# Kernel optimization log

Hardware: AMD Instinct MI355X
Metric: run time of the kernel (lower is better)

Reference implementation:

```python
import jax, jax.numpy as jnp
import numpy as np

B, S, D = 4, 2048, 1024  # batch, seq_len, input_dimension
KD, VD = 1024, 1024      # key_dim, value_dim


def setup_inputs() -> dict:
    key = jax.random.key(0)
    ks = jax.random.split(key, 9)
    sc_in = 1.0 / np.sqrt(D)
    sc_v = 1.0 / np.sqrt(VD)
    return {
        "x":  jax.random.normal(ks[0], (B, S, D), dtype=jnp.float32),
        "Wq": jax.random.normal(ks[1], (KD, D), dtype=jnp.float32) * sc_in,
        "bq": jax.random.normal(ks[2], (KD,), dtype=jnp.float32) * 0.01,
        "Wk": jax.random.normal(ks[3], (KD, D), dtype=jnp.float32) * sc_in,
        "bk": jax.random.normal(ks[4], (KD,), dtype=jnp.float32) * 0.01,
        "Wv": jax.random.normal(ks[5], (VD, D), dtype=jnp.float32) * sc_in,
        "bv": jax.random.normal(ks[6], (VD,), dtype=jnp.float32) * 0.01,
        "Wo": jax.random.normal(ks[7], (D, VD), dtype=jnp.float32) * sc_v,
        "bo": jax.random.normal(ks[8], (D,), dtype=jnp.float32) * 0.01,
    }


def reference(x, Wq, bq, Wk, bk, Wv, bv, Wo, bo):
    # projections (torch Linear: x @ W.T + b)
    q = jnp.einsum('bsd,kd->bsk', x, Wq) + bq   # (B,S,KD)
    k = jnp.einsum('bsd,kd->bsk', x, Wk) + bk   # (B,S,KD)
    v = jnp.einsum('bsd,vd->bsv', x, Wv) + bv   # (B,S,VD)

    scores = jnp.einsum('bqk,bsk->bqs', q, k) / jnp.sqrt(jnp.float32(KD))  # (B,S,S)

    # sign rescale: scores * sign(scores) (sign(0) mapped to 1) == |scores| with zeros kept
    sign_mask = jnp.sign(scores)
    sign_mask = sign_mask + (sign_mask == 0).astype(jnp.float32)

    # causal mask: lower-triangular (incl diag) multiplied by 1, strict upper -> -inf
    seq = scores.shape[-1]
    causal = jnp.tril(jnp.ones((seq, seq), dtype=bool))
    masked = jnp.where(causal, scores * sign_mask, -jnp.inf)

    weights = jax.nn.softmax(masked, axis=2)            # (B,S,S)
    out = jnp.einsum('bqs,bsv->bqv', weights, v)        # (B,S,VD)
    return jnp.einsum('bqv,dv->bqd', out, Wo) + bo      # (B,S,D)
```

## Files before the change

### kernel.cpp

```cpp
#include <hip/hip_runtime.h>
#include <hip/hip_bf16.h>
#include <cstdint>


#define BM 128
#define BN 128

typedef __attribute__((ext_vector_type(8))) __bf16 bf16x8;
typedef __attribute__((ext_vector_type(4))) __bf16 bf16x4;
typedef __attribute__((ext_vector_type(4))) float floatx4;

struct WPtr3 { const __bf16* w[3]; };
struct BPtr3 { const float* b[3]; };
struct Ptr3 { const float* p[3]; };

__device__ __forceinline__ void async_copy16(const __bf16* g, const __bf16* l) {
  __builtin_amdgcn_global_load_lds(
      (const __attribute__((address_space(1))) unsigned int*)(const void*)g,
      (__attribute__((address_space(3))) unsigned int*)(unsigned)(uintptr_t)(const void*)l,
      16, 0, 0);
}

__device__ __forceinline__ void gemm_core(const __bf16* __restrict__ pA,
                                          const __bf16* __restrict__ pB,
                                          int K, int kSteps64, int mb, int nb,
                                          floatx4 (&acc)[4][4]) {
  __shared__ __align__(16) __bf16 As0[BM * 32];
  __shared__ __align__(16) __bf16 As1[BM * 32];
  __shared__ __align__(16) __bf16 Bs0[BN * 32];
  __shared__ __align__(16) __bf16 Bs1[BN * 32];

  const int t = threadIdx.x;
  const int lane = t & 63;
  const int wave = t >> 6;
  const int quad = lane >> 4;
  const int l16 = lane & 15;
  const int wm = wave >> 1;
  const int wn = wave & 1;

  const __bf16* gA = pA + (long)(mb * BM + (t >> 2)) * K + ((t & 3) * 8);
  const __bf16* gB = pB + (long)(nb * BN + (t >> 2)) * K + ((t & 3) * 8);
  const long rowHalf = (long)64 * K;
  __bf16* lA0 = &As0[t * 8];
  __bf16* lA1 = &As1[t * 8];
  __bf16* lB0 = &Bs0[t * 8];
  __bf16* lB1 = &Bs1[t * 8];

  for (int kk = 0; kk < kSteps64; ++kk) {
    const long ko = (long)kk * 64;
    async_copy16(gA + ko, lA0);
    async_copy16(gA + ko + rowHalf, lA0 + 2048);
    async_copy16(gA + ko + 32, lA1);
    async_copy16(gA + ko + 32 + rowHalf, lA1 + 2048);
    async_copy16(gB + ko, lB0);
    async_copy16(gB + ko + rowHalf, lB0 + 2048);
    async_copy16(gB + ko + 32, lB1);
    async_copy16(gB + ko + 32 + rowHalf, lB1 + 2048);
    __syncthreads();

#pragma unroll
    for (int p = 0; p < 2; ++p) {
      const __bf16* As = p ? As1 : As0;
      const __bf16* Bs = p ? Bs1 : Bs0;
      bf16x8 af[4], bfr[4];
#pragma unroll
      for (int i = 0; i < 4; ++i) {
        af[i] = *(const bf16x8*)&As[(wm * 64 + i * 16 + l16) * 32 + quad * 8];
        bfr[i] = *(const bf16x8*)&Bs[(wn * 64 + i * 16 + l16) * 32 + quad * 8];
      }
#pragma unroll
      for (int i = 0; i < 4; ++i)
#pragma unroll
        for (int j = 0; j < 4; ++j)
          acc[i][j] = __builtin_amdgcn_mfma_f32_16x16x32_bf16(af[i], bfr[j],
                                                              acc[i][j], 0, 0, 0);
    }
    __syncthreads();
  }
}

__global__ void __launch_bounds__(256, 2)
gemm_wvo(const __bf16* __restrict__ Wob, const __bf16* __restrict__ Wvt,
         __bf16* __restrict__ Wvo) {
  const int id = blockIdx.x;
  const int mb = id >> 3, nb = id & 7;
  floatx4 acc[4][4] = {};
  gemm_core(Wob, Wvt, 1024, 16, mb, nb, acc);

  const int t = threadIdx.x;
  const int lane = t & 63, wave = t >> 6;
  const int rb = (wave >> 1) * 64 + (lane >> 4) * 4;
  const int cb = (wave & 1) * 64 + (lane & 15);
#pragma unroll
  for (int j4 = 0; j4 < 4; ++j4) {
    const int gc = nb * BN + cb + j4 * 16;
#pragma unroll
    for (int i = 0; i < 4; ++i) {
      const int gr = mb * BM + rb + i * 16;
#pragma unroll
      for (int r = 0; r < 4; ++r)
        Wvo[(long)(gr + r) * 1024 + gc] = (__bf16)acc[i][j4][r];
    }
  }
}

__global__ void __launch_bounds__(256, 2)
gemm_qku(const __bf16* __restrict__ xb, WPtr3 wgt, BPtr3 bias,
         __bf16* __restrict__ qk, __bf16* __restrict__ Ut,
         int S, int D, int KD, int B) {
  const int id = blockIdx.x;
  const int xcd = id & 7;
  const int j = id >> 3;
  const int mb = xcd * 8 + (j & 7);
  const int rest = j >> 3;
  const int nb = rest & 7;
  const int z = rest >> 3;

  floatx4 acc[4][4] = {};
  gemm_core(xb, wgt.w[z], D, D / 64, mb, nb, acc);

  const int t = threadIdx.x;
  const int lane = t & 63, wave = t >> 6;
  const int rb = (wave >> 1) * 64 + (lane >> 4) * 4;
  const int cb = (wave & 1) * 64 + (lane & 15);
  const float* bz = bias.b[z];

  if (z < 2) {
    __bf16* C = qk + (long)z * B * S * KD;
#pragma unroll
    for (int j4 = 0; j4 < 4; ++j4) {
      const int gc = nb * BN + cb + j4 * 16;
      const float bv = bz[gc];
#pragma unroll
      for (int i = 0; i < 4; ++i) {
        const int gr = mb * BM + rb + i * 16;
#pragma unroll
        for (int r = 0; r < 4; ++r)
          C[(long)(gr + r) * KD + gc] = (__bf16)(acc[i][j4][r] + bv);
      }
    }
  } else {
    const int bb = (mb * BM) / S;
    const int s0 = mb * BM - bb * S;
#pragma unroll
    for (int j4 = 0; j4 < 4; ++j4) {
      const int gc = nb * BN + cb + j4 * 16;
      const float bv = bz[gc];
#pragma unroll
      for (int i = 0; i < 4; ++i) {
        const int sr = s0 + rb + i * 16;
        bf16x4 o;
#pragma unroll
        for (int r = 0; r < 4; ++r) o[r] = (__bf16)(acc[i][j4][r] + bv);
        *(bf16x4*)&Ut[((long)bb * D + gc) * S + sr] = o;
      }
    }
  }
}

__global__ void __launch_bounds__(256, 2)
gemm_scores(const __bf16* __restrict__ q, const __bf16* __restrict__ k,
            __bf16* __restrict__ P, float* __restrict__ lsum, int S, int KD) {
  const int id = blockIdx.x;
  const int xcd = id & 7;
  const int j = id >> 3;
  const int nb = j & 15;
  const int comb = j >> 4;
  const int b = comb >> 1;
  const int mb = (comb & 1) ? (15 - xcd) : xcd;
  if (nb > mb) return;

  floatx4 acc[4][4] = {};
  gemm_core(q + (long)b * S * KD, k + (long)b * S * KD, KD, KD / 64, mb, nb, acc);

  const int t = threadIdx.x;
  const int lane = t & 63, wave = t >> 6;
  const int l16 = lane & 15;
  const int rb = (wave >> 1) * 64 + (lane >> 4) * 4;
  const int cb = (wave & 1) * 64 + l16;
  __bf16* C = P + (long)b * S * S;
  float* lrow = lsum + (long)b * S;
  const float sc = 0.03125f;

#pragma unroll
  for (int i = 0; i < 4; ++i) {
#pragma unroll
    for (int r = 0; r < 4; ++r) {
      const int row = mb * BM + rb + i * 16 + r;
      float psum = 0.f;
#pragma unroll
      for (int j4 = 0; j4 < 4; ++j4) {
        const int col = nb * BN + cb + j4 * 16;
        const float p = (col <= row) ? __expf(fabsf(acc[i][j4][r] * sc)) : 0.f;
        psum += p;
        C[(long)row * S + col] = (__bf16)p;
      }
      psum += __shfl_xor(psum, 1, 64);
      psum += __shfl_xor(psum, 2, 64);
      psum += __shfl_xor(psum, 4, 64);
      psum += __shfl_xor(psum, 8, 64);
      if (l16 == 0) atomicAdd(&lrow[row], psum);
    }
  }
}

__global__ void __launch_bounds__(256, 2)
gemm_pvo(const __bf16* __restrict__ P, const __bf16* __restrict__ Ut,
         const float* __restrict__ lsum, const float* __restrict__ bo,
         float* __restrict__ out, int S, int D) {
  const int id = blockIdx.x;
  const int xcd = id & 7;
  const int j = id >> 3;
  const int nb = j & 7;
  const int comb = j >> 3;
  const int b = comb >> 1;
  const int mb = (comb & 1) ? (15 - xcd) : xcd;

  floatx4 acc[4][4] = {};
  gemm_core(P + (long)b * S * S, Ut + (long)b * D * S, S, (mb + 1) * 2, mb, nb,
            acc);

  const int t = threadIdx.x;
  const int lane = t & 63, wave = t >> 6;
  const int rb = (wave >> 1) * 64 + (lane >> 4) * 4;
  const int cb = (wave & 1) * 64 + (lane & 15);
  const float* lrow = lsum + (long)b * S;

#pragma unroll
  for (int i = 0; i < 4; ++i) {
#pragma unroll
    for (int r = 0; r < 4; ++r) {
      const int row = mb * BM + rb + i * 16 + r;
      const float inv = 1.f / lrow[row];
#pragma unroll
      for (int j4 = 0; j4 < 4; ++j4) {
        const int col = nb * BN + cb + j4 * 16;
        out[((long)b * S + row) * D + col] = acc[i][j4][r] * inv + bo[col];
      }
    }
  }
}

__global__ void prep(const float* __restrict__ x, Ptr3 wp,
                     const float* __restrict__ Wv, const float* __restrict__ bv,
                     __bf16* __restrict__ xb, __bf16* __restrict__ Wb,
                     __bf16* __restrict__ Wvt, float* __restrict__ bvo,
                     float* __restrict__ lsum) {
  __shared__ __bf16 tile[64][66];
  __shared__ float wsum[4];
  const int bid = blockIdx.x;
  const int t = threadIdx.x;
  if (bid < 8192) {
    const long i = ((long)bid * 256 + t) * 4;
    const float4 f = *(const float4*)(x + i);
    bf16x4 o;
    o[0] = (__bf16)f.x; o[1] = (__bf16)f.y; o[2] = (__bf16)f.z; o[3] = (__bf16)f.w;
    *(bf16x4*)(xb + i) = o;
  } else if (bid < 11264) {
    const int slot = (bid - 8192) * 256 + t;
    const int which = slot >> 18;
    const long e = (long)(slot & 0x3ffff) * 4;
    const float4 f = *(const float4*)(wp.p[which] + e);
    bf16x4 o;
    o[0] = (__bf16)f.x; o[1] = (__bf16)f.y; o[2] = (__bf16)f.z; o[3] = (__bf16)f.w;
    *(bf16x4*)(Wb + ((long)which << 20) + e) = o;
  } else if (bid < 11520) {
    const int idx = bid - 11264;
    const int r0 = (idx >> 4) * 64, c0 = (idx & 15) * 64;
#pragma unroll
    for (int e = 0; e < 16; ++e) {
      const int i = e * 256 + t;
      const int r = i >> 6, c = i & 63;
      tile[r][c] = (__bf16)Wv[(long)(r0 + r) * 1024 + (c0 + c)];
    }
    __syncthreads();
#pragma unroll
    for (int e = 0; e < 16; ++e) {
      const int i = e * 256 + t;
      const int r = i >> 6, c = i & 63;
      Wvt[(long)(c0 + r) * 1024 + (r0 + c)] = tile[c][r];
    }
  } else if (bid < 12544) {
    const int d = bid - 11520;
    const float* row = wp.p[2] + (long)d * 1024;
    float s = 0.f;
    for (int v = t; v < 1024; v += 256) s += bv[v] * row[v];
#pragma unroll
    for (int off = 32; off > 0; off >>= 1) s += __shfl_down(s, off, 64);
    if ((t & 63) == 0) wsum[t >> 6] = s;
    __syncthreads();
    if (t == 0) bvo[d] = wsum[0] + wsum[1] + wsum[2] + wsum[3];
  } else {
#pragma unroll
    for (int e = 0; e < 8; ++e)
      *(float4*)(lsum + (e * 256 + t) * 4) = float4{0.f, 0.f, 0.f, 0.f};
  }
}

extern "C" void kernel_launch(void* const* d_in, const int* in_sizes, int n_in,
                              void* d_out, int out_size, void* d_ws, size_t ws_size,
                              hipStream_t stream) {
  const float* x = (const float*)d_in[0];
  const float* Wq = (const float*)d_in[1];
  const float* bq = (const float*)d_in[2];
  const float* Wk = (const float*)d_in[3];
  const float* bk = (const float*)d_in[4];
  const float* Wv = (const float*)d_in[5];
  const float* bv = (const float*)d_in[6];
  const float* Wo = (const float*)d_in[7];
  const float* bo = (const float*)d_in[8];
  float* out = (float*)d_out;

  constexpr int B = 4, S = 2048, D = 1024, KD = 1024;
  constexpr long MB_ = 1024 * 1024;

  char* w = (char*)d_ws;
  __bf16* xb = (__bf16*)(w);
  __bf16* qk = (__bf16*)(w + 16 * MB_);
  __bf16* Ut = (__bf16*)(w + 48 * MB_);
  __bf16* P  = (__bf16*)(w + 64 * MB_);
  __bf16* Wb = (__bf16*)(w + 96 * MB_);
  __bf16* Wvt = (__bf16*)(w + 102 * MB_);
  __bf16* Wvo = (__bf16*)(w + 104 * MB_);
  float* lsum = (float*)(w + 106 * MB_);
  float* bvo = (float*)(w + 106 * MB_ + 65536);

  __bf16* Wqb = Wb;
  __bf16* Wkb = Wb + (1l << 20);
  __bf16* Wob = Wb + (2l << 20);

  Ptr3 wp{{Wq, Wk, Wo}};
  prep<<<12545, 256, 0, stream>>>(x, wp, Wv, bv, xb, Wb, Wvt, bvo, lsum);

  gemm_wvo<<<64, 256, 0, stream>>>(Wob, Wvt, Wvo);

  WPtr3 w3{{Wqb, Wkb, Wvo}};
  BPtr3 b3{{bq, bk, bvo}};
  gemm_qku<<<1536, 256, 0, stream>>>(xb, w3, b3, qk, Ut, S, D, KD, B);

  gemm_scores<<<1024, 256, 0, stream>>>(qk, qk + (long)B * S * KD, P, lsum, S, KD);

  gemm_pvo<<<512, 256, 0, stream>>>(P, Ut, lsum, bo, out, S, D);
}
```

Before: 261.0 us.

## Split-K the causal PV·Wo GEMM into fixed-size K chunks with atomic accumulation

The final P×(V·Wo) GEMM previously gave each block a K range proportional to its row-block index, so causal triangular work was badly imbalanced across 512 blocks. It now splits K into chunks of 8 steps (512 columns), launching 1280 blocks that each handle one chunk and atomically add partial results into a zeroed output, with the bias added only by the first chunk. This adds a memset of the output and fp32 atomic traffic, and makes the summation order nondeterministic.

Result: slower. 320.0 us (+22.6%).

```diff
diff --git a/kernel.cpp b/kernel.cpp
--- a/kernel.cpp
+++ b/kernel.cpp
@@ -23,8 +23,8 @@
 
 __device__ __forceinline__ void gemm_core(const __bf16* __restrict__ pA,
                                           const __bf16* __restrict__ pB,
-                                          int K, int kSteps64, int mb, int nb,
-                                          floatx4 (&acc)[4][4]) {
+                                          int K, int kBeg, int kEnd, int mb,
+                                          int nb, floatx4 (&acc)[4][4]) {
   __shared__ __align__(16) __bf16 As0[BM * 32];
   __shared__ __align__(16) __bf16 As1[BM * 32];
   __shared__ __align__(16) __bf16 Bs0[BN * 32];
@@ -46,7 +46,7 @@
   __bf16* lB0 = &Bs0[t * 8];
   __bf16* lB1 = &Bs1[t * 8];
 
-  for (int kk = 0; kk < kSteps64; ++kk) {
+  for (int kk = kBeg; kk < kEnd; ++kk) {
     const long ko = (long)kk * 64;
     async_copy16(gA + ko, lA0);
     async_copy16(gA + ko + rowHalf, lA0 + 2048);
@@ -85,7 +85,7 @@
   const int id = blockIdx.x;
   const int mb = id >> 3, nb = id & 7;
   floatx4 acc[4][4] = {};
-  gemm_core(Wob, Wvt, 1024, 16, mb, nb, acc);
+  gemm_core(Wob, Wvt, 1024, 0, 16, mb, nb, acc);
 
   const int t = threadIdx.x;
   const int lane = t & 63, wave = t >> 6;
@@ -117,7 +117,7 @@
   const int z = rest >> 3;
 
   floatx4 acc[4][4] = {};
-  gemm_core(xb, wgt.w[z], D, D / 64, mb, nb, acc);
+  gemm_core(xb, wgt.w[z], D, 0, D / 64, mb, nb, acc);
 
   const int t = threadIdx.x;
   const int lane = t & 63, wave = t >> 6;
@@ -171,7 +171,8 @@
   if (nb > mb) return;
 
   floatx4 acc[4][4] = {};
-  gemm_core(q + (long)b * S * KD, k + (long)b * S * KD, KD, KD / 64, mb, nb, acc);
+  gemm_core(q + (long)b * S * KD, k + (long)b * S * KD, KD, 0, KD / 64, mb, nb,
+            acc);
 
   const int t = threadIdx.x;
   const int lane = t & 63, wave = t >> 6;
@@ -211,13 +212,18 @@
   const int id = blockIdx.x;
   const int xcd = id & 7;
   const int j = id >> 3;
-  const int nb = j & 7;
-  const int comb = j >> 3;
-  const int b = comb >> 1;
-  const int mb = (comb & 1) ? (15 - xcd) : xcd;
+  const int b = j / 40;
+  const int rem = j - b * 40;
+  const int nb = rem & 7;
+  const int ci = rem >> 3;
+  const int nchx = (2 * xcd + 9) >> 3;
+  const int mb = (ci < nchx) ? xcd : (15 - xcd);
+  const int ch = (ci < nchx) ? ci : (ci - nchx);
+  const int kBeg = ch * 8;
+  const int kEnd = min(kBeg + 8, 2 * (mb + 1));
 
   floatx4 acc[4][4] = {};
-  gemm_core(P + (long)b * S * S, Ut + (long)b * D * S, S, (mb + 1) * 2, mb, nb,
+  gemm_core(P + (long)b * S * S, Ut + (long)b * D * S, S, kBeg, kEnd, mb, nb,
             acc);
 
   const int t = threadIdx.x;
@@ -235,7 +241,8 @@
 #pragma unroll
       for (int j4 = 0; j4 < 4; ++j4) {
         const int col = nb * BN + cb + j4 * 16;
-        out[((long)b * S + row) * D + col] = acc[i][j4][r] * inv + bo[col];
+        const float add = acc[i][j4][r] * inv + (ch == 0 ? bo[col] : 0.f);
+        atomicAdd(&out[((long)b * S + row) * D + col], add);
       }
     }
   }
@@ -329,6 +336,8 @@
   __bf16* Wkb = Wb + (1l << 20);
   __bf16* Wob = Wb + (2l << 20);
 
+  hipMemsetAsync(out, 0, (long)B * S * D * sizeof(float), stream);
+
   Ptr3 wp{{Wq, Wk, Wo}};
   prep<<<12545, 256, 0, stream>>>(x, wp, Wv, bv, xb, Wb, Wvt, bvo, lsum);
 
@@ -340,5 +349,5 @@
 
   gemm_scores<<<1024, 256, 0, stream>>>(qk, qk + (long)B * S * KD, P, lsum, S, KD);
 
-  gemm_pvo<<<512, 256, 0, stream>>>(P, Ut, lsum, bo, out, S, D);
-}
+  gemm_pvo<<<1280, 256, 0, stream>>>(P, Ut, lsum, bo, out, S, D);
+}
```

## Use 128x64 tiles for scores and PV GEMMs with dense causal block enumeration

Applied to the files above, without the earlier changes.

Templates the shared GEMM core on the N-tile width and switches the scores and P·(Wv·Wo) kernels to 128x64 tiles. The scores kernel now enumerates only the causal (lower-triangular) 128x64 tiles with no early-exit blocks, and the PV kernel launches twice as many blocks. The goal is better load balance and occupancy on the triangular workloads and less idle launch overhead. In exchange, each block reuses A less, so L2/global traffic per FLOP rises.

Measured after the change: 266.9 us. 2.3% more time.

```diff
diff --git a/kernel.cpp b/kernel.cpp
--- a/kernel.cpp
+++ b/kernel.cpp
@@ -4,7 +4,6 @@
 
 
 #define BM 128
-#define BN 128
 
 typedef __attribute__((ext_vector_type(8))) __bf16 bf16x8;
 typedef __attribute__((ext_vector_type(4))) __bf16 bf16x4;
@@ -21,14 +20,16 @@
       16, 0, 0);
 }
 
+template <int JW>
 __device__ __forceinline__ void gemm_core(const __bf16* __restrict__ pA,
                                           const __bf16* __restrict__ pB,
-                                          int K, int kSteps64, int mb, int nb,
-                                          floatx4 (&acc)[4][4]) {
+                                          int K, int kBeg, int kEnd, int mb,
+                                          int nb, floatx4 (&acc)[4][JW]) {
+  constexpr int BN_ = JW * 32;
   __shared__ __align__(16) __bf16 As0[BM * 32];
   __shared__ __align__(16) __bf16 As1[BM * 32];
-  __shared__ __align__(16) __bf16 Bs0[BN * 32];
-  __shared__ __align__(16) __bf16 Bs1[BN * 32];
+  __shared__ __align__(16) __bf16 Bs0[BN_ * 32];
+  __shared__ __align__(16) __bf16 Bs1[BN_ * 32];
 
   const int t = threadIdx.x;
   const int lane = t & 63;
@@ -39,39 +40,43 @@
   const int wn = wave & 1;
 
   const __bf16* gA = pA + (long)(mb * BM + (t >> 2)) * K + ((t & 3) * 8);
-  const __bf16* gB = pB + (long)(nb * BN + (t >> 2)) * K + ((t & 3) * 8);
+  const __bf16* gB = pB + (long)(nb * BN_ + (t >> 2)) * K + ((t & 3) * 8);
   const long rowHalf = (long)64 * K;
   __bf16* lA0 = &As0[t * 8];
   __bf16* lA1 = &As1[t * 8];
   __bf16* lB0 = &Bs0[t * 8];
   __bf16* lB1 = &Bs1[t * 8];
 
-  for (int kk = 0; kk < kSteps64; ++kk) {
+  for (int kk = kBeg; kk < kEnd; ++kk) {
     const long ko = (long)kk * 64;
     async_copy16(gA + ko, lA0);
     async_copy16(gA + ko + rowHalf, lA0 + 2048);
     async_copy16(gA + ko + 32, lA1);
     async_copy16(gA + ko + 32 + rowHalf, lA1 + 2048);
     async_copy16(gB + ko, lB0);
-    async_copy16(gB + ko + rowHalf, lB0 + 2048);
     async_copy16(gB + ko + 32, lB1);
-    async_copy16(gB + ko + 32 + rowHalf, lB1 + 2048);
+    if (JW == 4) {
+      async_copy16(gB + ko + rowHalf, lB0 + 2048);
+      async_copy16(gB + ko + 32 + rowHalf, lB1 + 2048);
+    }
     __syncthreads();
 
 #pragma unroll
     for (int p = 0; p < 2; ++p) {
       const __bf16* As = p ? As1 : As0;
       const __bf16* Bs = p ? Bs1 : Bs0;
-      bf16x8 af[4], bfr[4];
-#pragma unroll
-      for (int i = 0; i < 4; ++i) {
+      bf16x8 af[4], bfr[JW];
+#pragma unroll
+      for (int i = 0; i < 4; ++i)
         af[i] = *(const bf16x8*)&As[(wm * 64 + i * 16 + l16) * 32 + quad * 8];
-        bfr[i] = *(const bf16x8*)&Bs[(wn * 64 + i * 16 + l16) * 32 + quad * 8];
-      }
+#pragma unroll
+      for (int j = 0; j < JW; ++j)
+        bfr[j] =
+            *(const bf16x8*)&Bs[(wn * (JW * 16) + j * 16 + l16) * 32 + quad * 8];
 #pragma unroll
       for (int i = 0; i < 4; ++i)
 #pragma unroll
-        for (int j = 0; j < 4; ++j)
+        for (int j = 0; j < JW; ++j)
           acc[i][j] = __builtin_amdgcn_mfma_f32_16x16x32_bf16(af[i], bfr[j],
                                                               acc[i][j], 0, 0, 0);
     }
@@ -85,7 +90,7 @@
   const int id = blockIdx.x;
   const int mb = id >> 3, nb = id & 7;
   floatx4 acc[4][4] = {};
-  gemm_core(Wob, Wvt, 1024, 16, mb, nb, acc);
+  gemm_core<4>(Wob, Wvt, 1024, 0, 16, mb, nb, acc);
 
   const int t = threadIdx.x;
   const int lane = t & 63, wave = t >> 6;
@@ -93,7 +98,7 @@
   const int cb = (wave & 1) * 64 + (lane & 15);
 #pragma unroll
   for (int j4 = 0; j4 < 4; ++j4) {
-    const int gc = nb * BN + cb + j4 * 16;
+    const int gc = nb * 128 + cb + j4 * 16;
 #pragma unroll
     for (int i = 0; i < 4; ++i) {
       const int gr = mb * BM + rb + i * 16;
@@ -117,7 +122,7 @@
   const int z = rest >> 3;
 
   floatx4 acc[4][4] = {};
-  gemm_core(xb, wgt.w[z], D, D / 64, mb, nb, acc);
+  gemm_core<4>(xb, wgt.w[z], D, 0, D / 64, mb, nb, acc);
 
   const int t = threadIdx.x;
   const int lane = t & 63, wave = t >> 6;
@@ -129,7 +134,7 @@
     __bf16* C = qk + (long)z * B * S * KD;
 #pragma unroll
     for (int j4 = 0; j4 < 4; ++j4) {
-      const int gc = nb * BN + cb + j4 * 16;
+      const int gc = nb * 128 + cb + j4 * 16;
       const float bv = bz[gc];
 #pragma unroll
       for (int i = 0; i < 4; ++i) {
@@ -144,7 +149,7 @@
     const int s0 = mb * BM - bb * S;
 #pragma unroll
     for (int j4 = 0; j4 < 4; ++j4) {
-      const int gc = nb * BN + cb + j4 * 16;
+      const int gc = nb * 128 + cb + j4 * 16;
       const float bv = bz[gc];
 #pragma unroll
       for (int i = 0; i < 4; ++i) {
@@ -164,20 +169,21 @@
   const int id = blockIdx.x;
   const int xcd = id & 7;
   const int j = id >> 3;
-  const int nb = j & 15;
-  const int comb = j >> 4;
-  const int b = comb >> 1;
-  const int mb = (comb & 1) ? (15 - xcd) : xcd;
-  if (nb > mb) return;
-
-  floatx4 acc[4][4] = {};
-  gemm_core(q + (long)b * S * KD, k + (long)b * S * KD, KD, KD / 64, mb, nb, acc);
+  const int b = j / 34;
+  const int ci = j - b * 34;
+  const int n1 = 2 * xcd + 2;
+  const int mb = (ci < n1) ? xcd : (15 - xcd);
+  const int nb = (ci < n1) ? ci : (ci - n1);
+
+  floatx4 acc[4][2] = {};
+  gemm_core<2>(q + (long)b * S * KD, k + (long)b * S * KD, KD, 0, KD / 64, mb,
+               nb, acc);
 
   const int t = threadIdx.x;
   const int lane = t & 63, wave = t >> 6;
   const int l16 = lane & 15;
   const int rb = (wave >> 1) * 64 + (lane >> 4) * 4;
-  const int cb = (wave & 1) * 64 + l16;
+  const int cb = (wave & 1) * 32 + l16;
   __bf16* C = P + (long)b * S * S;
   float* lrow = lsum + (long)b * S;
   const float sc = 0.03125f;
@@ -189,8 +195,8 @@
       const int row = mb * BM + rb + i * 16 + r;
       float psum = 0.f;
 #pragma unroll
-      for (int j4 = 0; j4 < 4; ++j4) {
-        const int col = nb * BN + cb + j4 * 16;
+      for (int j4 = 0; j4 < 2; ++j4) {
+        const int col = nb * 64 + cb + j4 * 16;
         const float p = (col <= row) ? __expf(fabsf(acc[i][j4][r] * sc)) : 0.f;
         psum += p;
         C[(long)row * S + col] = (__bf16)p;
@@ -211,19 +217,19 @@
   const int id = blockIdx.x;
   const int xcd = id & 7;
   const int j = id >> 3;
-  const int nb = j & 7;
-  const int comb = j >> 3;
-  const int b = comb >> 1;
-  const int mb = (comb & 1) ? (15 - xcd) : xcd;
-
-  floatx4 acc[4][4] = {};
-  gemm_core(P + (long)b * S * S, Ut + (long)b * D * S, S, (mb + 1) * 2, mb, nb,
-            acc);
+  const int b = j >> 5;
+  const int rem = j & 31;
+  const int nb = rem & 15;
+  const int mb = (rem >> 4) ? (15 - xcd) : xcd;
+
+  floatx4 acc[4][2] = {};
+  gemm_core<2>(P + (long)b * S * S, Ut + (long)b * D * S, S, 0, 2 * (mb + 1),
+               mb, nb, acc);
 
   const int t = threadIdx.x;
   const int lane = t & 63, wave = t >> 6;
   const int rb = (wave >> 1) * 64 + (lane >> 4) * 4;
-  const int cb = (wave & 1) * 64 + (lane & 15);
+  const int cb = (wave & 1) * 32 + (lane & 15);
   const float* lrow = lsum + (long)b * S;
 
 #pragma unroll
@@ -233,8 +239,8 @@
       const int row = mb * BM + rb + i * 16 + r;
       const float inv = 1.f / lrow[row];
 #pragma unroll
-      for (int j4 = 0; j4 < 4; ++j4) {
-        const int col = nb * BN + cb + j4 * 16;
+      for (int j4 = 0; j4 < 2; ++j4) {
+        const int col = nb * 64 + cb + j4 * 16;
         out[((long)b * S + row) * D + col] = acc[i][j4][r] * inv + bo[col];
       }
     }
@@ -338,7 +344,7 @@
   BPtr3 b3{{bq, bk, bvo}};
   gemm_qku<<<1536, 256, 0, stream>>>(xb, w3, b3, qk, Ut, S, D, KD, B);
 
-  gemm_scores<<<1024, 256, 0, stream>>>(qk, qk + (long)B * S * KD, P, lsum, S, KD);
-
-  gemm_pvo<<<512, 256, 0, stream>>>(P, Ut, lsum, bo, out, S, D);
-}
+  gemm_scores<<<1088, 256, 0, stream>>>(qk, qk + (long)B * S * KD, P, lsum, S, KD);
+
+  gemm_pvo<<<1024, 256, 0, stream>>>(P, Ut, lsum, bo, out, S, D);
+}
```

## Merge GEMM launches into two fused grids and compact causal score tiles

Applied to the files above, without the earlier changes.

Reorganizes the kernel schedule. The Wo·Wv weight-fusion GEMM now runs in the same launch as the Q/K projections, and the U projection (x·Wvo) shares a launch with the causal score GEMM, so independent work overlaps and the launch count drops. The score grid now enumerates only lower-triangular tiles (17 per XCD pair) instead of launching blocks that return immediately. The pvo block ordering is also remapped. The risk is that branch divergence inside a fused kernel causes register/occupancy imbalance, and that load balance across the mixed grids gets worse.

After: 248.6 us. -4.8%, faster.

```diff
diff --git a/kernel.cpp b/kernel.cpp
--- a/kernel.cpp
+++ b/kernel.cpp
@@ -4,14 +4,11 @@
 
 
 #define BM 128
-#define BN 128
 
 typedef __attribute__((ext_vector_type(8))) __bf16 bf16x8;
 typedef __attribute__((ext_vector_type(4))) __bf16 bf16x4;
 typedef __attribute__((ext_vector_type(4))) float floatx4;
 
-struct WPtr3 { const __bf16* w[3]; };
-struct BPtr3 { const float* b[3]; };
 struct Ptr3 { const float* p[3]; };
 
 __device__ __forceinline__ void async_copy16(const __bf16* g, const __bf16* l) {
@@ -23,12 +20,12 @@
 
 __device__ __forceinline__ void gemm_core(const __bf16* __restrict__ pA,
                                           const __bf16* __restrict__ pB,
-                                          int K, int kSteps64, int mb, int nb,
-                                          floatx4 (&acc)[4][4]) {
+                                          int K, int kBeg, int kEnd, int mb,
+                                          int nb, floatx4 (&acc)[4][4]) {
   __shared__ __align__(16) __bf16 As0[BM * 32];
   __shared__ __align__(16) __bf16 As1[BM * 32];
-  __shared__ __align__(16) __bf16 Bs0[BN * 32];
-  __shared__ __align__(16) __bf16 Bs1[BN * 32];
+  __shared__ __align__(16) __bf16 Bs0[BM * 32];
+  __shared__ __align__(16) __bf16 Bs1[BM * 32];
 
   const int t = threadIdx.x;
   const int lane = t & 63;
@@ -39,14 +36,14 @@
   const int wn = wave & 1;
 
   const __bf16* gA = pA + (long)(mb * BM + (t >> 2)) * K + ((t & 3) * 8);
-  const __bf16* gB = pB + (long)(nb * BN + (t >> 2)) * K + ((t & 3) * 8);
+  const __bf16* gB = pB + (long)(nb * BM + (t >> 2)) * K + ((t & 3) * 8);
   const long rowHalf = (long)64 * K;
   __bf16* lA0 = &As0[t * 8];
   __bf16* lA1 = &As1[t * 8];
   __bf16* lB0 = &Bs0[t * 8];
   __bf16* lB1 = &Bs1[t * 8];
 
-  for (int kk = 0; kk < kSteps64; ++kk) {
+  for (int kk = kBeg; kk < kEnd; ++kk) {
     const long ko = (long)kk * 64;
     async_copy16(gA + ko, lA0);
     async_copy16(gA + ko + rowHalf, lA0 + 2048);
@@ -80,56 +77,46 @@
 }
 
 __global__ void __launch_bounds__(256, 2)
-gemm_wvo(const __bf16* __restrict__ Wob, const __bf16* __restrict__ Wvt,
-         __bf16* __restrict__ Wvo) {
+fusedA(const __bf16* __restrict__ xb, const __bf16* __restrict__ Wb,
+       const float* __restrict__ bq, const float* __restrict__ bk,
+       __bf16* __restrict__ qk, const __bf16* __restrict__ Wob,
+       const __bf16* __restrict__ Wvt, __bf16* __restrict__ Wvo,
+       int S, int KD, int B) {
   const int id = blockIdx.x;
-  const int mb = id >> 3, nb = id & 7;
+  const __bf16 *pA, *pB;
+  int mb, nb, z;
+  if (id < 1024) {
+    const int xcd = id & 7;
+    const int j = id >> 3;
+    mb = xcd * 8 + (j & 7);
+    const int rest = j >> 3;
+    nb = rest & 7;
+    z = rest >> 3;
+    pA = xb;
+    pB = Wb + ((long)z << 20);
+  } else {
+    const int wid = id - 1024;
+    mb = wid >> 3;
+    nb = wid & 7;
+    z = 2;
+    pA = Wob;
+    pB = Wvt;
+  }
+
   floatx4 acc[4][4] = {};
-  gemm_core(Wob, Wvt, 1024, 16, mb, nb, acc);
+  gemm_core(pA, pB, KD, 0, KD / 64, mb, nb, acc);
 
   const int t = threadIdx.x;
   const int lane = t & 63, wave = t >> 6;
   const int rb = (wave >> 1) * 64 + (lane >> 4) * 4;
   const int cb = (wave & 1) * 64 + (lane & 15);
-#pragma unroll
-  for (int j4 = 0; j4 < 4; ++j4) {
-    const int gc = nb * BN + cb + j4 * 16;
-#pragma unroll
-    for (int i = 0; i < 4; ++i) {
-      const int gr = mb * BM + rb + i * 16;
-#pragma unroll
-      for (int r = 0; r < 4; ++r)
-        Wvo[(long)(gr + r) * 1024 + gc] = (__bf16)acc[i][j4][r];
-    }
-  }
-}
-
-__global__ void __launch_bounds__(256, 2)
-gemm_qku(const __bf16* __restrict__ xb, WPtr3 wgt, BPtr3 bias,
-         __bf16* __restrict__ qk, __bf16* __restrict__ Ut,
-         int S, int D, int KD, int B) {
-  const int id = blockIdx.x;
-  const int xcd = id & 7;
-  const int j = id >> 3;
-  const int mb = xcd * 8 + (j & 7);
-  const int rest = j >> 3;
-  const int nb = rest & 7;
-  const int z = rest >> 3;
-
-  floatx4 acc[4][4] = {};
-  gemm_core(xb, wgt.w[z], D, D / 64, mb, nb, acc);
-
-  const int t = threadIdx.x;
-  const int lane = t & 63, wave = t >> 6;
-  const int rb = (wave >> 1) * 64 + (lane >> 4) * 4;
-  const int cb = (wave & 1) * 64 + (lane & 15);
-  const float* bz = bias.b[z];
 
   if (z < 2) {
     __bf16* C = qk + (long)z * B * S * KD;
+    const float* bz = z ? bk : bq;
 #pragma unroll
     for (int j4 = 0; j4 < 4; ++j4) {
-      const int gc = nb * BN + cb + j4 * 16;
+      const int gc = nb * 128 + cb + j4 * 16;
       const float bv = bz[gc];
 #pragma unroll
       for (int i = 0; i < 4; ++i) {
@@ -140,66 +127,100 @@
       }
     }
   } else {
-    const int bb = (mb * BM) / S;
-    const int s0 = mb * BM - bb * S;
 #pragma unroll
     for (int j4 = 0; j4 < 4; ++j4) {
-      const int gc = nb * BN + cb + j4 * 16;
-      const float bv = bz[gc];
+      const int gc = nb * 128 + cb + j4 * 16;
 #pragma unroll
       for (int i = 0; i < 4; ++i) {
-        const int sr = s0 + rb + i * 16;
-        bf16x4 o;
-#pragma unroll
-        for (int r = 0; r < 4; ++r) o[r] = (__bf16)(acc[i][j4][r] + bv);
-        *(bf16x4*)&Ut[((long)bb * D + gc) * S + sr] = o;
+        const int gr = mb * BM + rb + i * 16;
+#pragma unroll
+        for (int r = 0; r < 4; ++r)
+          Wvo[(long)(gr + r) * 1024 + gc] = (__bf16)acc[i][j4][r];
       }
     }
   }
 }
 
 __global__ void __launch_bounds__(256, 2)
-gemm_scores(const __bf16* __restrict__ q, const __bf16* __restrict__ k,
-            __bf16* __restrict__ P, float* __restrict__ lsum, int S, int KD) {
+fusedB(const __bf16* __restrict__ xb, const __bf16* __restrict__ Wvo,
+       const float* __restrict__ bvo, __bf16* __restrict__ Ut,
+       const __bf16* __restrict__ q, const __bf16* __restrict__ k,
+       __bf16* __restrict__ P, float* __restrict__ lsum,
+       int S, int KD, int D) {
   const int id = blockIdx.x;
-  const int xcd = id & 7;
-  const int j = id >> 3;
-  const int nb = j & 15;
-  const int comb = j >> 4;
-  const int b = comb >> 1;
-  const int mb = (comb & 1) ? (15 - xcd) : xcd;
-  if (nb > mb) return;
+  const __bf16 *pA, *pB;
+  int mb, nb, b, mode;
+  if (id < 512) {
+    const int xcd = id & 7;
+    const int j = id >> 3;
+    mb = xcd * 8 + (j & 7);
+    nb = j >> 3;
+    b = 0;
+    mode = 0;
+    pA = xb;
+    pB = Wvo;
+  } else {
+    const int sid = id - 512;
+    const int xcd = sid & 7;
+    const int r = sid >> 3;
+    b = r / 17;
+    const int ci = r - b * 17;
+    const int n1 = xcd + 1;
+    mb = (ci < n1) ? xcd : (15 - xcd);
+    nb = (ci < n1) ? ci : (ci - n1);
+    mode = 1;
+    pA = q + (long)b * S * KD;
+    pB = k + (long)b * S * KD;
+  }
 
   floatx4 acc[4][4] = {};
-  gemm_core(q + (long)b * S * KD, k + (long)b * S * KD, KD, KD / 64, mb, nb, acc);
+  gemm_core(pA, pB, KD, 0, KD / 64, mb, nb, acc);
 
   const int t = threadIdx.x;
   const int lane = t & 63, wave = t >> 6;
   const int l16 = lane & 15;
   const int rb = (wave >> 1) * 64 + (lane >> 4) * 4;
   const int cb = (wave & 1) * 64 + l16;
-  __bf16* C = P + (long)b * S * S;
-  float* lrow = lsum + (long)b * S;
-  const float sc = 0.03125f;
-
-#pragma unroll
-  for (int i = 0; i < 4; ++i) {
-#pragma unroll
-    for (int r = 0; r < 4; ++r) {
-      const int row = mb * BM + rb + i * 16 + r;
-      float psum = 0.f;
-#pragma unroll
-      for (int j4 = 0; j4 < 4; ++j4) {
-        const int col = nb * BN + cb + j4 * 16;
-        const float p = (col <= row) ? __expf(fabsf(acc[i][j4][r] * sc)) : 0.f;
-        psum += p;
-        C[(long)row * S + col] = (__bf16)p;
-      }
-      psum += __shfl_xor(psum, 1, 64);
-      psum += __shfl_xor(psum, 2, 64);
-      psum += __shfl_xor(psum, 4, 64);
-      psum += __shfl_xor(psum, 8, 64);
-      if (l16 == 0) atomicAdd(&lrow[row], psum);
+
+  if (mode == 0) {
+    const int bb = (mb * BM) / S;
+    const int s0 = mb * BM - bb * S;
+#pragma unroll
+    for (int j4 = 0; j4 < 4; ++j4) {
+      const int gc = nb * 128 + cb + j4 * 16;
+      const float bv = bvo[gc];
+#pragma unroll
+      for (int i = 0; i < 4; ++i) {
+        const int sr = s0 + rb + i * 16;
+        bf16x4 o;
+#pragma unroll
+        for (int r = 0; r < 4; ++r) o[r] = (__bf16)(acc[i][j4][r] + bv);
+        *(bf16x4*)&Ut[((long)bb * D + gc) * S + sr] = o;
+      }
+    }
+  } else {
+    __bf16* C = P + (long)b * S * S;
+    float* lrow = lsum + (long)b * S;
+    const float sc = 0.03125f;
+#pragma unroll
+    for (int i = 0; i < 4; ++i) {
+#pragma unroll
+      for (int r = 0; r < 4; ++r) {
+        const int row = mb * BM + rb + i * 16 + r;
+        float psum = 0.f;
+#pragma unroll
+        for (int j4 = 0; j4 < 4; ++j4) {
+          const int col = nb * 128 + cb + j4 * 16;
+          const float p = (col <= row) ? __expf(fabsf(acc[i][j4][r] * sc)) : 0.f;
+          psum += p;
+          C[(long)row * S + col] = (__bf16)p;
+        }
+        psum += __shfl_xor(psum, 1, 64);
+        psum += __shfl_xor(psum, 2, 64);
+        psum += __shfl_xor(psum, 4, 64);
+        psum += __shfl_xor(psum, 8, 64);
+        if (l16 == 0) atomicAdd(&lrow[row], psum);
+      }
     }
   }
 }
@@ -211,14 +232,15 @@
   const int id = blockIdx.x;
   const int xcd = id & 7;
   const int j = id >> 3;
-  const int nb = j & 7;
-  const int comb = j >> 3;
-  const int b = comb >> 1;
-  const int mb = (comb & 1) ? (15 - xcd) : xcd;
+  const int half = j >> 5;
+  const int idx = j & 31;
+  const int b = idx >> 3;
+  const int nb = idx & 7;
+  const int mb = half ? xcd : (15 - xcd);
 
   floatx4 acc[4][4] = {};
-  gemm_core(P + (long)b * S * S, Ut + (long)b * D * S, S, (mb + 1) * 2, mb, nb,
-            acc);
+  gemm_core(P + (long)b * S * S, Ut + (long)b * D * S, S, 0, 2 * (mb + 1), mb,
+            nb, acc);
 
   const int t = threadIdx.x;
   const int lane = t & 63, wave = t >> 6;
@@ -234,7 +256,7 @@
       const float inv = 1.f / lrow[row];
 #pragma unroll
       for (int j4 = 0; j4 < 4; ++j4) {
-        const int col = nb * BN + cb + j4 * 16;
+        const int col = nb * 128 + cb + j4 * 16;
         out[((long)b * S + row) * D + col] = acc[i][j4][r] * inv + bo[col];
       }
     }
@@ -325,20 +347,15 @@
   float* lsum = (float*)(w + 106 * MB_);
   float* bvo = (float*)(w + 106 * MB_ + 65536);
 
-  __bf16* Wqb = Wb;
-  __bf16* Wkb = Wb + (1l << 20);
   __bf16* Wob = Wb + (2l << 20);
 
   Ptr3 wp{{Wq, Wk, Wo}};
   prep<<<12545, 256, 0, stream>>>(x, wp, Wv, bv, xb, Wb, Wvt, bvo, lsum);
 
-  gemm_wvo<<<64, 256, 0, stream>>>(Wob, Wvt, Wvo);
-
-  WPtr3 w3{{Wqb, Wkb, Wvo}};
-  BPtr3 b3{{bq, bk, bvo}};
-  gemm_qku<<<1536, 256, 0, stream>>>(xb, w3, b3, qk, Ut, S, D, KD, B);
-
-  gemm_scores<<<1024, 256, 0, stream>>>(qk, qk + (long)B * S * KD, P, lsum, S, KD);
+  fusedA<<<1088, 256, 0, stream>>>(xb, Wb, bq, bk, qk, Wob, Wvt, Wvo, S, KD, B);
+
+  fusedB<<<1056, 256, 0, stream>>>(xb, Wvo, bvo, Ut, qk, qk + (long)B * S * KD,
+                                   P, lsum, S, KD, D);
 
   gemm_pvo<<<512, 256, 0, stream>>>(P, Ut, lsum, bo, out, S, D);
 }
```
